# Kernel tuning notes

Measured on AMD Instinct MI355X. Metric: run time of the kernel, lower is better.

Reference implementation:

```python
import jax, jax.numpy as jnp
import numpy as np

B, H, W, C = 4, 64, 64, 96
EXPAND = 2
D_INNER = EXPAND * C  # 192
N = 16   # d_state
K = 4    # scan directions
DT_RANK = int(np.ceil(C / 16))  # 6


def setup_inputs() -> dict:
    key = jax.random.key(0)
    ks = jax.random.split(key, 8)
    def rn(k, shape, scale=0.02):
        return jax.random.normal(k, shape, dtype=jnp.float32) * scale
    return {
        "x": jax.random.normal(ks[0], (B, H, W, C), dtype=jnp.float32),
        "ln_g": jnp.ones((C,), jnp.float32),
        "ln_b": jnp.zeros((C,), jnp.float32),
        "in_proj_w": rn(ks[1], (C, 2 * D_INNER)),
        "in_proj_b": jnp.zeros((2 * D_INNER,), jnp.float32),
        "conv_w": rn(ks[2], (D_INNER, 1, 3, 3), 0.1),
        "conv_b": jnp.zeros((D_INNER,), jnp.float32),
        "x_proj_w": rn(ks[3], (K, DT_RANK + 2 * N, D_INNER)),
        "dt_proj_w": rn(ks[4], (K, D_INNER, DT_RANK), 0.1),
        "dt_proj_b": rn(ks[5], (K, D_INNER), 0.1),
        "A_logs": jnp.log(jnp.tile(jnp.arange(1, N + 1, dtype=jnp.float32)[None, :], (K * D_INNER, 1))),
        "Ds": jnp.ones((K * D_INNER,), jnp.float32),
        "out_norm_g": jnp.ones((D_INNER,), jnp.float32),
        "out_norm_b": jnp.zeros((D_INNER,), jnp.float32),
        "out_proj_w": rn(ks[6], (D_INNER, C)),
        "out_proj_b": jnp.zeros((C,), jnp.float32),
    }


def _ln(x, g, b, eps):
    mu = x.mean(-1, keepdims=True)
    var = jnp.mean((x - mu) ** 2, axis=-1, keepdims=True)
    return (x - mu) * jax.lax.rsqrt(var + eps) * g + b


def _vss_forward(x, ln_g, ln_b, in_proj_w, in_proj_b, conv_w, conv_b,
                 x_proj_w, dt_proj_w, dt_proj_b, A_logs, Ds,
                 out_norm_g, out_norm_b, out_proj_w, out_proj_b):
    Bb, Hh, Ww, Cc = x.shape
    L = Hh * Ww
    d = D_INNER
    # ln_1 (eps=1e-6), then SS2D on channels-first layout
    xn = _ln(x, ln_g, ln_b, 1e-6)
    xz = jnp.einsum('bhwc,ce->bhwe', xn, in_proj_w) + in_proj_b
    xi, z = jnp.split(xz, 2, axis=-1)
    xi = xi.transpose(0, 3, 1, 2)  # (B, d, H, W)
    xi = jax.lax.conv_general_dilated(
        xi, conv_w, (1, 1), 'SAME', feature_group_count=d,
        dimension_numbers=('NCHW', 'OIHW', 'NCHW'))
    xi = jax.nn.silu(xi + conv_b[None, :, None, None])
    # 4 scan directions: row-major, col-major, and their reverses
    x_hw = xi.reshape(Bb, d, L)
    x_wh = xi.transpose(0, 1, 3, 2).reshape(Bb, d, L)
    xs = jnp.stack([x_hw, x_wh], axis=1)                      # (B,2,d,L)
    xs = jnp.concatenate([xs, jnp.flip(xs, axis=-1)], axis=1)  # (B,K,d,L)
    x_dbl = jnp.einsum('bkdl,kcd->bkcl', xs, x_proj_w)         # (B,K,R+2N,L)
    dt_r = x_dbl[:, :, :DT_RANK]
    Bs = x_dbl[:, :, DT_RANK:DT_RANK + N]                      # (B,K,N,L)
    Cs = x_dbl[:, :, DT_RANK + N:]                             # (B,K,N,L)
    dts = jnp.einsum('bkrl,kdr->bkdl', dt_r, dt_proj_w)
    dts = jax.nn.softplus(dts + dt_proj_b[None, :, :, None])
    A = -jnp.exp(A_logs).reshape(K, d, N)
    Dsk = Ds.reshape(K, d)

    def step(h, inp):
        u_t, dt_t, B_t, C_t = inp                  # (B,K,d),(B,K,d),(B,K,N),(B,K,N)
        dA = jnp.exp(dt_t[..., None] * A)          # (B,K,d,N)
        h = dA * h + (dt_t * u_t)[..., None] * B_t[:, :, None, :]
        y = jnp.einsum('bkdn,bkn->bkd', h, C_t)
        return h, y

    seq = (xs.transpose(3, 0, 1, 2), dts.transpose(3, 0, 1, 2),
           Bs.transpose(3, 0, 1, 2), Cs.transpose(3, 0, 1, 2))
    h0 = jnp.zeros((Bb, K, d, N), xs.dtype)
    _, ys = jax.lax.scan(step, h0, seq)            # ys: (L,B,K,d)
    ys = ys.transpose(1, 2, 3, 0)                  # (B,K,d,L)
    ys = ys + Dsk[None, :, :, None] * xs
    # merge the 4 directions back into one row-major map
    inv_y = jnp.flip(ys[:, 2:4], axis=-1)
    wh_y = ys[:, 1].reshape(Bb, d, Ww, Hh).transpose(0, 1, 3, 2).reshape(Bb, d, L)
    invwh_y = inv_y[:, 1].reshape(Bb, d, Ww, Hh).transpose(0, 1, 3, 2).reshape(Bb, d, L)
    y = ys[:, 0] + inv_y[:, 0] + wh_y + invwh_y    # (B,d,L)
    y = y.transpose(0, 2, 1).reshape(Bb, Hh, Ww, d)
    y = _ln(y, out_norm_g, out_norm_b, 1e-5)
    y = y * jax.nn.silu(z)
    out = jnp.einsum('bhwd,dc->bhwc', y, out_proj_w) + out_proj_b
    return x + out  # residual (drop_path = 0 -> identity)


def reference(x, ln_g, ln_b, in_proj_w, in_proj_b, conv_w, conv_b, x_proj_w,
              dt_proj_w, dt_proj_b, A_logs, Ds, out_norm_g, out_norm_b,
              out_proj_w, out_proj_b):
    return _vss_forward(x, ln_g, ln_b, in_proj_w, in_proj_b, conv_w, conv_b,
                        x_proj_w, dt_proj_w, dt_proj_b, A_logs, Ds,
                        out_norm_g, out_norm_b, out_proj_w, out_proj_b)
```

## Files before the change

### kernel.cpp

```cpp
#include <hip/hip_runtime.h>
#include <math.h>

#define CC   96
#define DIN  192
#define NST  16
#define KDIR 4
#define DTR  6
#define LL   4096
#define BB   4
#define NSEG 128
#define SEGLEN 32
#define XROW 40

#define SZ_BLD ((long)BB*LL*DIN)

__device__ __forceinline__ float sigmoidf_(float x){
    return __builtin_amdgcn_rcpf(1.0f + __expf(-x));
}
__device__ __forceinline__ int whmap(int l){ return ((l & 63) << 6) | (l >> 6); }

__device__ __forceinline__ void dt_and_E(float s, float& dt, float& E){
    const float LOG2E = 1.4426950408889634f;
    const float LN2   = 0.6931471805599453f;
    float sn  = s * LOG2E;
    float t   = __builtin_amdgcn_exp2f(-fabsf(sn));
    float opt = 1.0f + t;
    float r   = __builtin_amdgcn_rcpf(opt);
    E  = (s > 0.f) ? t*r : r;
    dt = LN2 * (fmaxf(sn, 0.f) + __builtin_amdgcn_logf(opt));
}
__device__ __forceinline__ void pow_tree(float E, float* En){
    En[0]=E;
    float E2=E*E;        En[1]=E2;
    En[2]=E2*E;  float E4=E2*E2; En[3]=E4;
    En[4]=E4*E;  En[5]=E4*E2;  En[6]=E4*En[2];
    float E8=E4*E4;      En[7]=E8;
    En[8]=E8*E;  En[9]=E8*E2;  En[10]=E8*En[2]; En[11]=E8*E4;
    En[12]=E8*En[4]; En[13]=E8*En[5]; En[14]=E8*En[6]; En[15]=E8*E8;
}
__device__ __forceinline__ void dir_base(int k, int lg0, int& p0, int& stride){
    switch(k & 3){
        case 0:  p0 = lg0;               stride = 1;   break;
        case 1:  p0 = whmap(lg0);        stride = 64;  break;
        case 2:  p0 = LL - 1 - lg0;      stride = -1;  break;
        default: p0 = whmap(LL-1-lg0);   stride = -64; break;
    }
}

__global__ __launch_bounds__(256) void kT(const float* __restrict__ xw,
                                          float* __restrict__ xwt)
{
    int tid = blockIdx.x*256 + threadIdx.x;
    if(tid >= KDIR*38*192) return;
    int d  = tid % 192;
    int kc = tid / 192;
    int k  = kc / 38, c = kc % 38;
    xwt[((long)k*192 + d)*38 + c] = xw[tid];
}

__global__ __launch_bounds__(192) void kA(const float* __restrict__ x,
        const float* __restrict__ lng, const float* __restrict__ lnb,
        const float* __restrict__ W,   const float* __restrict__ bias,
        float* __restrict__ xi, float* __restrict__ z)
{
    __shared__ float xn[16*96];
    __shared__ float sc1[192], sc2[192];
    __shared__ float mu[16], rs[16];
    int t = threadIdx.x;
    long row0 = (long)blockIdx.x * 16;

    for(int q=t; q<16*96; q+=192) xn[q] = x[row0*96 + q];
    __syncthreads();
    {
        int r = t/12, i = t%12;
        float4 v0 = *(const float4*)(&xn[r*96 + i*8]);
        float4 v1 = *(const float4*)(&xn[r*96 + i*8 + 4]);
        float s  = v0.x+v0.y+v0.z+v0.w + v1.x+v1.y+v1.z+v1.w;
        float ss = v0.x*v0.x+v0.y*v0.y+v0.z*v0.z+v0.w*v0.w
                 + v1.x*v1.x+v1.y*v1.y+v1.z*v1.z+v1.w*v1.w;
        sc1[t]=s; sc2[t]=ss;
        __syncthreads();
        if(t<16){
            float S=0.f, SS=0.f;
            for(int j=0;j<12;j++){ S+=sc1[t*12+j]; SS+=sc2[t*12+j]; }
            float m = S*(1.0f/96.0f);
            float var = SS*(1.0f/96.0f) - m*m;
            mu[t]=m; rs[t]=rsqrtf(var + 1e-6f);
        }
        __syncthreads();
    }
    for(int q=t; q<16*96; q+=192){
        int r=q/96, c=q%96;
        xn[q] = (xn[q]-mu[r])*rs[r]*lng[c] + lnb[c];
    }
    __syncthreads();

    float acc0[16], acc1[16];
    #pragma unroll
    for(int r=0;r<16;r++){ acc0[r]=0.f; acc1[r]=0.f; }
    for(int c0=0; c0<96; c0+=4){
        float4 xv[16];
        #pragma unroll
        for(int r=0;r<16;r++) xv[r] = *(const float4*)(&xn[r*96 + c0]);
        #pragma unroll
        for(int j=0;j<4;j++){
            float w0 = W[(c0+j)*384 + t];
            float w1 = W[(c0+j)*384 + t + 192];
            #pragma unroll
            for(int r=0;r<16;r++){
                float xvj = (j==0)?xv[r].x:(j==1)?xv[r].y:(j==2)?xv[r].z:xv[r].w;
                acc0[r] = fmaf(xvj, w0, acc0[r]);
                acc1[r] = fmaf(xvj, w1, acc1[r]);
            }
        }
    }
    float b0 = bias[t], b1 = bias[t+192];
    #pragma unroll
    for(int r=0;r<16;r++){
        xi[(row0+r)*DIN + t] = acc0[r] + b0;
        z [(row0+r)*DIN + t] = acc1[r] + b1;
    }
}

__global__ __launch_bounds__(256) void kB(const float* __restrict__ xi,
        const float* __restrict__ cw, const float* __restrict__ cb,
        float* __restrict__ xc)
{
    long idx = (long)blockIdx.x*256 + threadIdx.x;
    if(idx >= SZ_BLD) return;
    int d = (int)(idx % DIN);
    long rg = idx / DIN;
    int p = (int)(rg % LL); int b = (int)(rg / LL);
    int h = p >> 6, w = p & 63;
    float acc = 0.f;
    #pragma unroll
    for(int dh=0; dh<3; dh++){
        int hh = h + dh - 1;
        if(hh < 0 || hh >= 64) continue;
        #pragma unroll
        for(int dw=0; dw<3; dw++){
            int ww2 = w + dw - 1;
            if(ww2 < 0 || ww2 >= 64) continue;
            acc = fmaf(xi[((long)b*LL + hh*64 + ww2)*DIN + d], cw[d*9 + dh*3 + dw], acc);
        }
    }
    acc += cb[d];
    xc[idx] = acc * sigmoidf_(acc);
}

__global__ __launch_bounds__(192) void kC(const float* __restrict__ xc,
        const float* __restrict__ xwt, float* __restrict__ xdbl)
{
    __shared__ float ls[8*192];
    int t = threadIdx.x;
    long row0 = (long)blockIdx.x * 8;
    int b  = (int)(row0 / LL);
    int p0 = (int)(row0 % LL);
    for(int q=t; q<8*192; q+=192) ls[q] = xc[row0*DIN + q];
    __syncthreads();
    if(t < 152){
        int k = t/38, c = t%38;
        const float* wt = xwt + (long)k*192*38 + c;
        float acc[8];
        #pragma unroll
        for(int r=0;r<8;r++) acc[r]=0.f;
        for(int d=0; d<192; d+=4){
            float w0 = wt[(d+0)*38];
            float w1 = wt[(d+1)*38];
            float w2 = wt[(d+2)*38];
            float w3 = wt[(d+3)*38];
            #pragma unroll
            for(int r=0;r<8;r++){
                float4 lv = *(const float4*)(&ls[r*192 + d]);
                acc[r] = fmaf(lv.x,w0, fmaf(lv.y,w1, fmaf(lv.z,w2, fmaf(lv.w,w3, acc[r]))));
            }
        }
        int cs = (c < 6) ? c : c + 2;
        #pragma unroll
        for(int r=0;r<8;r++){
            int p = p0 + r;
            int lk;
            if(k==0) lk = p;
            else if(k==1) lk = whmap(p);
            else if(k==2) lk = LL-1-p;
            else lk = LL-1-whmap(p);
            xdbl[(((long)(b*KDIR + k)*LL + lk)*XROW) + cs] = acc[r];
        }
    }
}

__global__ __launch_bounds__(192) void kD2(const float* __restrict__ xc,
        const float* __restrict__ xdbl, const float* __restrict__ alog,
        const float* __restrict__ dtw,  const float* __restrict__ dtb,
        float* __restrict__ hend, float* __restrict__ dtsum)
{
    __shared__ float rows[SEGLEN*XROW];
    int t = threadIdx.x;
    int blk = blockIdx.x;
    int bk = blk / NSEG, seg = blk % NSEG;
    int b = bk / KDIR, k = bk % KDIR;
    {
        const float* src = xdbl + ((long)bk*LL + seg*SEGLEN)*XROW;
        for(int q=t; q<SEGLEN*XROW; q+=192) rows[q] = src[q];
    }
    int d = t, kd = k*192 + d;
    float a[16]; bool fast = true;
    #pragma unroll
    for(int n=0;n<16;n++){
        a[n] = -__expf(alog[kd*16 + n]);
        fast = fast && (fabsf(a[n] + (float)(n+1)) < 1e-3f);
    }
    float w6[6];
    #pragma unroll
    for(int r=0;r<6;r++) w6[r] = dtw[kd*6 + r];
    float bdt = dtb[kd];

    int lg0 = seg * SEGLEN;
    int p0, stride; dir_base(k, lg0, p0, stride);
    long addr  = ((long)b*LL + p0)*DIN + d;
    long astep = (long)stride*DIN;

    float h[16];
    #pragma unroll
    for(int n=0;n<16;n++) h[n]=0.f;
    float sdt = 0.f;
    __syncthreads();

    float u = xc[addr];
    for(int i=0; i<SEGLEN; i++){
        const float* row = &rows[i*XROW];
        float s = bdt;
        #pragma unroll
        for(int r=0;r<6;r++) s = fmaf(row[r], w6[r], s);
        float dt, E; dt_and_E(s, dt, E);
        sdt += dt;
        float wi = dt * u;
        float unext = 0.f;
        long addrN = addr + astep;
        if(i+1 < SEGLEN) unext = xc[addrN];
        float En[16];
        if(fast){ pow_tree(E, En); }
        else {
            #pragma unroll
            for(int n=0;n<16;n++) En[n] = __expf(dt * a[n]);
        }
        float Bv[16];
        #pragma unroll
        for(int n=0;n<16;n+=4) *(float4*)(Bv+n) = *(const float4*)(row + 8 + n);
        #pragma unroll
        for(int n=0;n<16;n++) h[n] = fmaf(En[n], h[n], wi*Bv[n]);
        addr = addrN; u = unext;
    }
    long hb = (((long)bk*NSEG + seg)*192 + d)*16;
    #pragma unroll
    for(int n=0;n<16;n+=4)
        *(float4*)(&hend[hb+n]) = make_float4(h[n],h[n+1],h[n+2],h[n+3]);
    dtsum[((long)bk*NSEG + seg)*192 + d] = sdt;
}

__global__ __launch_bounds__(256) void kE3(const float* __restrict__ alog,
        const float* __restrict__ dtsum, float* __restrict__ hx)
{
    int tid = blockIdx.x*256 + threadIdx.x;
    int c     = tid & 15;
    int chain = tid >> 4;
    int n  = chain & 15;
    int d  = (chain >> 4) % 192;
    int bk = chain / 3072;
    int k  = bk & 3;
    float an = -__expf(alog[(k*192 + d)*16 + n]);
    long sbase = (long)bk*NSEG*192  + d;
    long hbase = (long)bk*NSEG*3072 + d*16 + n;
    int seg0 = c*8;

    float P[8], he[8];
    #pragma unroll
    for(int i=0;i<8;i++){
        float sd = dtsum[sbase + (long)(seg0+i)*192];
        he[i]    = hx[hbase + (long)(seg0+i)*3072];
        P[i]     = __expf(an * sd);
    }
    float Pc = 1.f, Hc = 0.f;
    #pragma unroll
    for(int i=0;i<8;i++){
        Hc = fmaf(P[i], Hc, he[i]);
        Pc *= P[i];
    }
    #pragma unroll
    for(int dist=1; dist<16; dist<<=1){
        float Pp = __shfl_up(Pc, dist, 16);
        float Hp = __shfl_up(Hc, dist, 16);
        if(c >= dist){
            Hc = fmaf(Pc, Hp, Hc);
            Pc *= Pp;
        }
    }
    float H = __shfl_up(Hc, 1, 16);
    if(c == 0) H = 0.f;
    #pragma unroll
    for(int i=0;i<8;i++){
        hx[hbase + (long)(seg0+i)*3072] = H;
        H = fmaf(P[i], H, he[i]);
    }
}

__global__ __launch_bounds__(192) void kF2(const float* __restrict__ xc,
        const float* __restrict__ xdbl, const float* __restrict__ alog,
        const float* __restrict__ dtw,  const float* __restrict__ dtb,
        const float* __restrict__ Ds,   const float* __restrict__ Hprev,
        float* __restrict__ ys0, float* __restrict__ ys123)
{
    __shared__ float rows[SEGLEN*XROW];
    int t = threadIdx.x;
    int blk = blockIdx.x;
    int bk = blk / NSEG, seg = blk % NSEG;
    int b = bk / KDIR, k = bk % KDIR;
    {
        const float* src = xdbl + ((long)bk*LL + seg*SEGLEN)*XROW;
        for(int q=t; q<SEGLEN*XROW; q+=192) rows[q] = src[q];
    }
    int d = t, kd = k*192 + d;
    float a[16]; bool fast = true;
    #pragma unroll
    for(int n=0;n<16;n++){
        a[n] = -__expf(alog[kd*16 + n]);
        fast = fast && (fabsf(a[n] + (float)(n+1)) < 1e-3f);
    }
    float w6[6];
    #pragma unroll
    for(int r=0;r<6;r++) w6[r] = dtw[kd*6 + r];
    float bdt = dtb[kd];
    float Dd  = Ds[kd];
    float h[16];
    long hb = (((long)bk*NSEG + seg)*192 + d)*16;
    #pragma unroll
    for(int n=0;n<16;n+=4){
        float4 v = *(const float4*)(&Hprev[hb+n]);
        h[n]=v.x; h[n+1]=v.y; h[n+2]=v.z; h[n+3]=v.w;
    }
    float* ybuf = (k==0) ? ys0 : (ys123 + (long)(k-1)*SZ_BLD);

    int lg0 = seg * SEGLEN;
    int p0, stride; dir_base(k, lg0, p0, stride);
    long addr  = ((long)b*LL + p0)*DIN + d;
    long astep = (long)stride*DIN;
    __syncthreads();

    float u = xc[addr];
    for(int i=0; i<SEGLEN; i++){
        const float* row = &rows[i*XROW];
        float s = bdt;
        #pragma unroll
        for(int r=0;r<6;r++) s = fmaf(row[r], w6[r], s);
        float dt, E; dt_and_E(s, dt, E);
        float wi = dt * u;
        float unext = 0.f;
        long addrN = addr + astep;
        if(i+1 < SEGLEN) unext = xc[addrN];
        float En[16];
        if(fast){ pow_tree(E, En); }
        else {
            #pragma unroll
            for(int n=0;n<16;n++) En[n] = __expf(dt * a[n]);
        }
        float Bv[16], Cv[16];
        #pragma unroll
        for(int n=0;n<16;n+=4){
            *(float4*)(Bv+n) = *(const float4*)(row + 8 + n);
            *(float4*)(Cv+n) = *(const float4*)(row + 24 + n);
        }
        float y = Dd * u;
        #pragma unroll
        for(int n=0;n<16;n++){
            h[n] = fmaf(En[n], h[n], wi*Bv[n]);
            y = fmaf(h[n], Cv[n], y);
        }
        ybuf[addr] = y;
        addr = addrN; u = unext;
    }
}

__global__ __launch_bounds__(384) void kG(const float* __restrict__ ys0,
        const float* __restrict__ ys123, const float* __restrict__ z,
        const float* __restrict__ ong, const float* __restrict__ onb,
        const float* __restrict__ Wout, const float* __restrict__ ob,
        const float* __restrict__ x, float* __restrict__ out)
{
    __shared__ float yb[16*192];
    __shared__ float sc1[384], sc2[384];
    __shared__ float mu[16], rs[16];
    int t = threadIdx.x;
    long row0 = (long)blockIdx.x * 16;

    for(int q=t; q<3072; q+=384){
        long off = row0*DIN + q;
        yb[q] = ys0[off] + ys123[off] + ys123[SZ_BLD + off] + ys123[2*SZ_BLD + off];
    }
    __syncthreads();
    {
        int r = t/24, i = t%24;
        float s=0.f, ss=0.f;
        #pragma unroll
        for(int j=0;j<8;j++){ float v = yb[r*192 + i*8 + j]; s+=v; ss+=v*v; }
        sc1[t]=s; sc2[t]=ss;
        __syncthreads();
        if(t<16){
            float S=0.f, SS=0.f;
            for(int j=0;j<24;j++){ S+=sc1[t*24+j]; SS+=sc2[t*24+j]; }
            float m = S*(1.0f/192.0f);
            float var = SS*(1.0f/192.0f) - m*m;
            mu[t]=m; rs[t]=rsqrtf(var + 1e-5f);
        }
        __syncthreads();
    }
    for(int q=t; q<3072; q+=384){
        int r=q/192, dd=q%192;
        float v = (yb[q]-mu[r])*rs[r]*ong[dd] + onb[dd];
        float zz = z[row0*DIN + q];
        yb[q] = v * (zz * sigmoidf_(zz));
    }
    __syncthreads();
    int c = t % 96, rg4 = t / 96;
    float acc[4] = {0.f,0.f,0.f,0.f};
    for(int dd=0; dd<192; dd++){
        float wv = Wout[dd*96 + c];
        #pragma unroll
        for(int j=0;j<4;j++) acc[j] = fmaf(yb[(rg4*4+j)*192 + dd], wv, acc[j]);
    }
    float bv = ob[c];
    for(int j=0;j<4;j++){
        long row = row0 + rg4*4 + j;
        out[row*96 + c] = x[row*96 + c] + acc[j] + bv;
    }
}

extern "C" void kernel_launch(void* const* d_in, const int* in_sizes, int n_in,
                              void* d_out, int out_size, void* d_ws, size_t ws_size,
                              hipStream_t stream)
{
    const float* x    = (const float*)d_in[0];
    const float* lng  = (const float*)d_in[1];
    const float* lnb  = (const float*)d_in[2];
    const float* ipw  = (const float*)d_in[3];
    const float* ipb  = (const float*)d_in[4];
    const float* cw   = (const float*)d_in[5];
    const float* cb   = (const float*)d_in[6];
    const float* xpw  = (const float*)d_in[7];
    const float* dtw  = (const float*)d_in[8];
    const float* dtb  = (const float*)d_in[9];
    const float* alog = (const float*)d_in[10];
    const float* Ds   = (const float*)d_in[11];
    const float* ong  = (const float*)d_in[12];
    const float* onb  = (const float*)d_in[13];
    const float* opw  = (const float*)d_in[14];
    const float* opb  = (const float*)d_in[15];

    float* ws    = (float*)d_ws;
    float* xi    = ws + 0;
    float* z     = ws + 3145728;
    float* xc    = ws + 6291456;
    float* xdbl  = ws + 9437184;
    float* ys123 = ws + 12058624;
    float* hx    = ws + 21495808;
    float* dtsum = ws + 27787264;
    float* xwt   = ws + 28180480;
    float* ys0   = xi;
    float* out   = (float*)d_out;

    hipLaunchKernelGGL(kT,  dim3(114),   dim3(256), 0, stream, xpw, xwt);
    hipLaunchKernelGGL(kA,  dim3(1024),  dim3(192), 0, stream, x, lng, lnb, ipw, ipb, xi, z);
    hipLaunchKernelGGL(kB,  dim3(12288), dim3(256), 0, stream, xi, cw, cb, xc);
    hipLaunchKernelGGL(kC,  dim3(2048),  dim3(192), 0, stream, xc, xwt, xdbl);
    hipLaunchKernelGGL(kD2, dim3(2048),  dim3(192), 0, stream, xc, xdbl, alog, dtw, dtb,
                       hx, dtsum);
    hipLaunchKernelGGL(kE3, dim3(3072),  dim3(256), 0, stream, alog, dtsum, hx);
    hipLaunchKernelGGL(kF2, dim3(2048),  dim3(192), 0, stream, xc, xdbl, alog, dtw, dtb,
                       Ds, hx, ys0, ys123);
    hipLaunchKernelGGL(kG,  dim3(1024),  dim3(384), 0, stream, ys0, ys123, z, ong, onb,
                       opw, opb, x, out);
}
```

Baseline: 312.1 us.

## Restructure x_proj kernel: per-wave rows, lane-per-output weights, drop shared memory

The x_proj weight transpose now stores weights as [d][152], so consecutive lanes read consecutive outputs and loads coalesce. kC drops the shared-memory staging and the block barrier. Each 64-lane wave handles 8 rows, with each lane computing up to 3 of the 152 outputs. The row data is read as wave-uniform float4 loads straight from global memory. This removes the idle threads (40 of 192 before) and the strided weight reads, at the cost of more registers and redundant global reads of each row across the three output groups.

```diff
diff --git a/kernel.cpp b/kernel.cpp
--- a/kernel.cpp
+++ b/kernel.cpp
@@ -54,8 +54,7 @@
     if(tid >= KDIR*38*192) return;
     int d  = tid % 192;
     int kc = tid / 192;
-    int k  = kc / 38, c = kc % 38;
-    xwt[((long)k*192 + d)*38 + c] = xw[tid];
+    xwt[(long)d*152 + kc] = xw[tid];
 }
 
 __global__ __launch_bounds__(192) void kA(const float* __restrict__ x,
@@ -148,43 +147,63 @@
     xc[idx] = acc * sigmoidf_(acc);
 }
 
-__global__ __launch_bounds__(192) void kC(const float* __restrict__ xc,
+__global__ __launch_bounds__(256) void kC(const float* __restrict__ xc,
         const float* __restrict__ xwt, float* __restrict__ xdbl)
 {
-    __shared__ float ls[8*192];
     int t = threadIdx.x;
-    long row0 = (long)blockIdx.x * 8;
+    int wave = t >> 6, l = t & 63;
+    long row0 = (long)blockIdx.x * 32 + wave * 8;
     int b  = (int)(row0 / LL);
     int p0 = (int)(row0 % LL);
-    for(int q=t; q<8*192; q+=192) ls[q] = xc[row0*DIN + q];
-    __syncthreads();
-    if(t < 152){
-        int k = t/38, c = t%38;
-        const float* wt = xwt + (long)k*192*38 + c;
-        float acc[8];
-        #pragma unroll
-        for(int r=0;r<8;r++) acc[r]=0.f;
-        for(int d=0; d<192; d+=4){
-            float w0 = wt[(d+0)*38];
-            float w1 = wt[(d+1)*38];
-            float w2 = wt[(d+2)*38];
-            float w3 = wt[(d+3)*38];
-            #pragma unroll
-            for(int r=0;r<8;r++){
-                float4 lv = *(const float4*)(&ls[r*192 + d]);
-                acc[r] = fmaf(lv.x,w0, fmaf(lv.y,w1, fmaf(lv.z,w2, fmaf(lv.w,w3, acc[r]))));
-            }
-        }
-        int cs = (c < 6) ? c : c + 2;
+    const float* rp = xc + row0 * DIN;
+
+    int c0 = l, c1 = 64 + l;
+    bool has2 = (l < 24);
+    int c2 = has2 ? (128 + l) : 0;
+
+    float acc0[8], acc1[8], acc2[8];
+    #pragma unroll
+    for(int r=0;r<8;r++){ acc0[r]=0.f; acc1[r]=0.f; acc2[r]=0.f; }
+
+    for(int d=0; d<192; d+=4){
+        float w0j[4], w1j[4], w2j[4];
+        #pragma unroll
+        for(int j=0;j<4;j++){
+            const float* wr = xwt + (long)(d+j)*152;
+            w0j[j] = wr[c0];
+            w1j[j] = wr[c1];
+            w2j[j] = wr[c2];
+        }
         #pragma unroll
         for(int r=0;r<8;r++){
-            int p = p0 + r;
-            int lk;
-            if(k==0) lk = p;
-            else if(k==1) lk = whmap(p);
-            else if(k==2) lk = LL-1-p;
-            else lk = LL-1-whmap(p);
-            xdbl[(((long)(b*KDIR + k)*LL + lk)*XROW) + cs] = acc[r];
+            float4 xv = *(const float4*)(rp + r*DIN + d);
+            acc0[r] = fmaf(xv.x,w0j[0], fmaf(xv.y,w0j[1], fmaf(xv.z,w0j[2], fmaf(xv.w,w0j[3], acc0[r]))));
+            acc1[r] = fmaf(xv.x,w1j[0], fmaf(xv.y,w1j[1], fmaf(xv.z,w1j[2], fmaf(xv.w,w1j[3], acc1[r]))));
+            acc2[r] = fmaf(xv.x,w2j[0], fmaf(xv.y,w2j[1], fmaf(xv.z,w2j[2], fmaf(xv.w,w2j[3], acc2[r]))));
+        }
+    }
+
+    #pragma unroll
+    for(int r=0;r<8;r++){
+        int p = p0 + r;
+        int lk0 = p, lk1 = whmap(p);
+        {
+            int k = c0/38, c = c0%38;
+            int cs = (c<6)? c : c+2;
+            int lk = (k==0)? lk0 : (k==1)? lk1 : (k==2)? (LL-1-lk0) : (LL-1-lk1);
+            xdbl[(((long)(b*KDIR + k)*LL + lk)*XROW) + cs] = acc0[r];
+        }
+        {
+            int k = c1/38, c = c1%38;
+            int cs = (c<6)? c : c+2;
+            int lk = (k==0)? lk0 : (k==1)? lk1 : (k==2)? (LL-1-lk0) : (LL-1-lk1);
+            xdbl[(((long)(b*KDIR + k)*LL + lk)*XROW) + cs] = acc1[r];
+        }
+        if(has2){
+            int k = c2/38, c = c2%38;
+            int cs = (c<6)? c : c+2;
+            int lk = (k==0)? lk0 : (k==1)? lk1 : (k==2)? (LL-1-lk0) : (LL-1-lk1);
+            xdbl[(((long)(b*KDIR + k)*LL + lk)*XROW) + cs] = acc2[r];
         }
     }
 }
@@ -470,7 +489,7 @@
     hipLaunchKernelGGL(kT,  dim3(114),   dim3(256), 0, stream, xpw, xwt);
     hipLaunchKernelGGL(kA,  dim3(1024),  dim3(192), 0, stream, x, lng, lnb, ipw, ipb, xi, z);
     hipLaunchKernelGGL(kB,  dim3(12288), dim3(256), 0, stream, xi, cw, cb, xc);
-    hipLaunchKernelGGL(kC,  dim3(2048),  dim3(192), 0, stream, xc, xwt, xdbl);
+    hipLaunchKernelGGL(kC,  dim3(512),   dim3(256), 0, stream, xc, xwt, xdbl);
     hipLaunchKernelGGL(kD2, dim3(2048),  dim3(192), 0, stream, xc, xdbl, alog, dtw, dtb,
                        hx, dtsum);
     hipLaunchKernelGGL(kE3, dim3(3072),  dim3(256), 0, stream, alog, dtsum, hx);
```

Measured after the change: 304.2 us. 1.03x faster.
